# Performance work log

Hardware: AMD Instinct MI355X
Metric: run time of the kernel (lower is better)

## Reference

```python
import jax, jax.numpy as jnp
import numpy as np

N = 500000   # num instances
C = 64       # num clock regions (8x8 grid)
CHIP_W, CHIP_H = 168.0, 480.0


def setup_inputs() -> dict:
    key = jax.random.key(0)
    k1, k2, k3 = jax.random.split(key, 3)
    # 8x8 grid of clock-region well boxes (xl, yl, xh, yh) tiling the chip
    gx, gy = 8, 8
    cw, ch = CHIP_W / gx, CHIP_H / gy
    ix = np.arange(C) % gx
    iy = np.arange(C) // gx
    well_boxes = jnp.asarray(
        np.stack([ix * cw, iy * ch, (ix + 1) * cw, (iy + 1) * ch], axis=1),
        dtype=jnp.float32)
    # instance centers uniformly over the chip
    inst_pos = jax.random.uniform(k1, (N, 2), dtype=jnp.float32) * jnp.array(
        [CHIP_W, CHIP_H], dtype=jnp.float32)
    # half sizes in [0.25, 0.75) sites (module stores inst_sizes * 0.5)
    half_inst_sizes = jax.random.uniform(k2, (N, 2), dtype=jnp.float32) * 0.5 + 0.25
    inst_areas = 4.0 * half_inst_sizes[:, 0] * half_inst_sizes[:, 1]
    # per-instance candidate CR availability; guarantee >=1 available CR
    avail = jax.random.randint(k3, (N, C), 0, 2) > 0
    avail = avail.at[:, 0].set(True)
    exponents = jnp.full((N,), 2.0, dtype=jnp.float32)
    return {
        'inst_pos': inst_pos,
        'half_inst_sizes': half_inst_sizes,
        'inst_areas': inst_areas,
        'well_boxes': well_boxes,
        'inst_cr_avail_map': avail,
        'exponents': exponents,
    }


def reference(inst_pos, half_inst_sizes, inst_areas, well_boxes,
              inst_cr_avail_map, exponents):
    # Per-instance CR selection + box-overlap well energy.
    x = inst_pos[:, 0:1]           # (N,1)
    y = inst_pos[:, 1:2]
    hx = half_inst_sizes[:, 0:1]
    hy = half_inst_sizes[:, 1:2]
    xl, yl, xh, yh = (well_boxes[:, 0], well_boxes[:, 1],
                      well_boxes[:, 2], well_boxes[:, 3])  # each (C,)
    # protrusion distance of the instance box outside each well box, (N,C)
    dx = jnp.maximum(jnp.maximum(xl - (x - hx), (x + hx) - xh), 0.0)
    dy = jnp.maximum(jnp.maximum(yl - (y - hy), (y + hy) - yh), 0.0)
    dist = dx + dy
    # mask out unavailable clock regions, pick nearest available CR
    dist = jnp.where(inst_cr_avail_map, dist, jnp.inf)
    selected_crs = jnp.argmin(dist, axis=1)  # (N,)
    dx_sel = jnp.take_along_axis(dx, selected_crs[:, None], axis=1)[:, 0]
    dy_sel = jnp.take_along_axis(dy, selected_crs[:, None], axis=1)[:, 0]
    # per-instance exponentiated well energy
    energy = jnp.power(dx_sel, exponents) + jnp.power(dy_sel, exponents)
    return energy
```

## Files before the change

### kernel.cpp

```cpp
#include <hip/hip_runtime.h>
#include <stdint.h>


#define C_WELLS 64

__global__ __launch_bounds__(256, 8)
void energy_well_kernel(const float* __restrict__ inst_pos,
                        const float* __restrict__ half_sizes,
                        const float* __restrict__ well_boxes,
                        const int*   __restrict__ avail,
                        const float* __restrict__ exponents,
                        float* __restrict__ out,
                        int N)
{
    const int lane = threadIdx.x & 63;
    int waveId = __builtin_amdgcn_readfirstlane(
        (int)((blockIdx.x * blockDim.x + threadIdx.x) >> 6));
    const int nWaves = (gridDim.x * blockDim.x) >> 6;

    const float4 box = ((const float4*)well_boxes)[lane];

    for (int i = waveId; i < N; i += nWaves) {
        const float x  = inst_pos[2 * i];
        const float y  = inst_pos[2 * i + 1];
        const float hx = half_sizes[2 * i];
        const float hy = half_sizes[2 * i + 1];
        const float e  = exponents[i];
        const int av = avail[(size_t)i * C_WELLS + lane];

        const float dx = fmaxf(fmaxf(box.x - (x - hx), (x + hx) - box.z), 0.0f);
        const float dy = fmaxf(fmaxf(box.y - (y - hy), (y + hy) - box.w), 0.0f);
        float dist = dx + dy;
        dist = av ? dist : __builtin_inff();

        float m = dist;
        #pragma unroll
        for (int off = 32; off >= 1; off >>= 1)
            m = fminf(m, __shfl_xor(m, off, 64));

        unsigned long long eq = __ballot(dist == m);
        const int w = __ffsll((long long)eq) - 1;

        const float dxs = __shfl(dx, w, 64);
        const float dys = __shfl(dy, w, 64);

        if (lane == 0) {
            float energy;
            if (e == 2.0f) {
                energy = dxs * dxs + dys * dys;
            } else {
                energy = powf(dxs, e) + powf(dys, e);
            }
            out[i] = energy;
        }
    }
}

extern "C" void kernel_launch(void* const* d_in, const int* in_sizes, int n_in,
                              void* d_out, int out_size, void* d_ws, size_t ws_size,
                              hipStream_t stream)
{
    const float* inst_pos   = (const float*)d_in[0];
    const float* half_sizes = (const float*)d_in[1];
    const float* well_boxes = (const float*)d_in[3];
    const int*   avail      = (const int*)d_in[4];
    const float* exponents  = (const float*)d_in[5];
    float* out = (float*)d_out;

    const int N = in_sizes[5];

    const int blocks = 2048;
    energy_well_kernel<<<dim3(blocks), dim3(256), 0, stream>>>(
        inst_pos, half_sizes, well_boxes, avail, exponents, out, N);
}
```

Before: 242.2 us.

## Process 64 instances per wave with ballot-packed availability masks

Switches from one instance per wave with cross-lane min reduction to one instance per lane, with each wave handling a tile of 64 instances. Availability rows are read coalesced and packed into per-lane 64-bit masks via ballot, then each lane scans all wells serially from broadcast box loads. This is meant to remove the per-instance shuffle reduction and serialized latency, increasing memory-level parallelism on the large availability array, at the cost of more per-lane ALU work.

After: 225.3 us. -7.0%, faster.

```diff
diff --git a/kernel.cpp b/kernel.cpp
--- a/kernel.cpp
+++ b/kernel.cpp
@@ -7,50 +7,65 @@
 __global__ __launch_bounds__(256, 8)
 void energy_well_kernel(const float* __restrict__ inst_pos,
                         const float* __restrict__ half_sizes,
-                        const float* __restrict__ well_boxes,
+                        const float4* __restrict__ well_boxes,
                         const int*   __restrict__ avail,
                         const float* __restrict__ exponents,
                         float* __restrict__ out,
-                        int N)
+                        int N, int nTiles)
 {
     const int lane = threadIdx.x & 63;
-    int waveId = __builtin_amdgcn_readfirstlane(
-        (int)((blockIdx.x * blockDim.x + threadIdx.x) >> 6));
+    const int waveId = (int)((blockIdx.x * blockDim.x + threadIdx.x) >> 6);
     const int nWaves = (gridDim.x * blockDim.x) >> 6;
 
-    const float4 box = ((const float4*)well_boxes)[lane];
+    for (int tile = waveId; tile < nTiles; tile += nWaves) {
+        const int base = tile << 6;
+        const int i    = base + lane;
 
-    for (int i = waveId; i < N; i += nWaves) {
-        const float x  = inst_pos[2 * i];
-        const float y  = inst_pos[2 * i + 1];
-        const float hx = half_sizes[2 * i];
-        const float hy = half_sizes[2 * i + 1];
-        const float e  = exponents[i];
-        const int av = avail[(size_t)i * C_WELLS + lane];
+        unsigned long long myMask = 0ull;
+        if (base + C_WELLS <= N) {
+            #pragma unroll 16
+            for (int j = 0; j < C_WELLS; ++j) {
+                const int av = avail[(size_t)(base + j) * C_WELLS + lane];
+                const unsigned long long m = __ballot(av != 0);
+                if (lane == j) myMask = m;
+            }
+        } else {
+            #pragma unroll 16
+            for (int j = 0; j < C_WELLS; ++j) {
+                int av = 0;
+                if (base + j < N) av = avail[(size_t)(base + j) * C_WELLS + lane];
+                const unsigned long long m = __ballot(av != 0);
+                if (lane == j) myMask = m;
+            }
+        }
 
-        const float dx = fmaxf(fmaxf(box.x - (x - hx), (x + hx) - box.z), 0.0f);
-        const float dy = fmaxf(fmaxf(box.y - (y - hy), (y + hy) - box.w), 0.0f);
-        float dist = dx + dy;
-        dist = av ? dist : __builtin_inff();
+        float x = 0.f, y = 0.f, hx = 0.f, hy = 0.f, e = 2.0f;
+        if (i < N) {
+            const float2 p = ((const float2*)inst_pos)[i];
+            const float2 h = ((const float2*)half_sizes)[i];
+            x = p.x; y = p.y; hx = h.x; hy = h.y;
+            e = exponents[i];
+        }
+        const float xm = x - hx, xp = x + hx;
+        const float ym = y - hy, yp = y + hy;
 
-        float m = dist;
+        float best = __builtin_inff();
+        float bdx = 0.0f, bdy = 0.0f;
         #pragma unroll
-        for (int off = 32; off >= 1; off >>= 1)
-            m = fminf(m, __shfl_xor(m, off, 64));
+        for (int c = 0; c < C_WELLS; ++c) {
+            const float4 box = well_boxes[c];
+            const float dx = fmaxf(fmaxf(box.x - xm, xp - box.z), 0.0f);
+            const float dy = fmaxf(fmaxf(box.y - ym, yp - box.w), 0.0f);
+            float dist = dx + dy;
+            const bool av = (myMask >> c) & 1ull;
+            dist = av ? dist : __builtin_inff();
+            if (dist < best) { best = dist; bdx = dx; bdy = dy; }
+        }
 
-        unsigned long long eq = __ballot(dist == m);
-        const int w = __ffsll((long long)eq) - 1;
-
-        const float dxs = __shfl(dx, w, 64);
-        const float dys = __shfl(dy, w, 64);
-
-        if (lane == 0) {
+        if (i < N) {
             float energy;
-            if (e == 2.0f) {
-                energy = dxs * dxs + dys * dys;
-            } else {
-                energy = powf(dxs, e) + powf(dys, e);
-            }
+            if (e == 2.0f) energy = bdx * bdx + bdy * bdy;
+            else           energy = powf(bdx, e) + powf(bdy, e);
             out[i] = energy;
         }
     }
@@ -60,16 +75,18 @@
                               void* d_out, int out_size, void* d_ws, size_t ws_size,
                               hipStream_t stream)
 {
-    const float* inst_pos   = (const float*)d_in[0];
-    const float* half_sizes = (const float*)d_in[1];
-    const float* well_boxes = (const float*)d_in[3];
-    const int*   avail      = (const int*)d_in[4];
-    const float* exponents  = (const float*)d_in[5];
+    const float*  inst_pos   = (const float*)d_in[0];
+    const float*  half_sizes = (const float*)d_in[1];
+    const float4* well_boxes = (const float4*)d_in[3];
+    const int*    avail      = (const int*)d_in[4];
+    const float*  exponents  = (const float*)d_in[5];
     float* out = (float*)d_out;
 
     const int N = in_sizes[5];
+    const int nTiles = (N + C_WELLS - 1) / C_WELLS;
+    const int wavesNeeded = nTiles;
+    const int blocks = (wavesNeeded + 3) / 4;
 
-    const int blocks = 2048;
     energy_well_kernel<<<dim3(blocks), dim3(256), 0, stream>>>(
-        inst_pos, half_sizes, well_boxes, avail, exponents, out, N);
+        inst_pos, half_sizes, well_boxes, avail, exponents, out, N, nTiles);
 }
```

## Process 16 instances per wave with vector avail loads and prefetch

Applied to the files above, without the earlier changes.

Each wave now handles 16 instances per tile, with 4 lanes per instance. Each lane loads 16 availability flags as four int4 loads and does a serial argmin over its 16 regions. A 4-lane shuffle reduction on a packed (distance, lane) key then picks the first minimum, replacing the 64-wide shuffle reduction per instance. The next tile's data is prefetched into registers while the current tile is computed. Grid size and occupancy hint are halved. The bandwidth-bound avail read becomes wider and is overlapped with compute, at the cost of more registers and a well-box layout hardcoded for the 8x8 grid.

New measurement: 199.2 us. -17.8%, faster.

```diff
diff --git a/kernel.cpp b/kernel.cpp
--- a/kernel.cpp
+++ b/kernel.cpp
@@ -4,55 +4,120 @@
 
 #define C_WELLS 64
 
-__global__ __launch_bounds__(256, 8)
-void energy_well_kernel(const float* __restrict__ inst_pos,
-                        const float* __restrict__ half_sizes,
-                        const float* __restrict__ well_boxes,
-                        const int*   __restrict__ avail,
-                        const float* __restrict__ exponents,
+struct TileWork {
+    int4   av[4];
+    float2 p, h;
+    float  e;
+};
+
+__device__ __forceinline__ TileWork load_tile(
+    const int4* __restrict__ avail4, const float2* __restrict__ inst_pos,
+    const float2* __restrict__ half_sizes, const float* __restrict__ exponents,
+    int tile, int lane, int N)
+{
+    TileWork w;
+    const int i  = tile * 16 + (lane >> 2);
+    const int ii = i < N ? i : N - 1;
+    const int4* a = avail4 + ((size_t)ii * 16 + (size_t)(lane & 3) * 4);
+    w.av[0] = a[0]; w.av[1] = a[1]; w.av[2] = a[2]; w.av[3] = a[3];
+    w.p = inst_pos[ii];
+    w.h = half_sizes[ii];
+    w.e = exponents[ii];
+    return w;
+}
+
+__global__ __launch_bounds__(256, 4)
+void energy_well_kernel(const float2* __restrict__ inst_pos,
+                        const float2* __restrict__ half_sizes,
+                        const float*  __restrict__ well_boxes,
+                        const int4*   __restrict__ avail4,
+                        const float*  __restrict__ exponents,
                         float* __restrict__ out,
-                        int N)
+                        int N, int nT16)
 {
     const int lane = threadIdx.x & 63;
-    int waveId = __builtin_amdgcn_readfirstlane(
-        (int)((blockIdx.x * blockDim.x + threadIdx.x) >> 6));
+    const int sub  = lane & 3;
+    const int waveId = (int)((blockIdx.x * blockDim.x + threadIdx.x) >> 6);
     const int nWaves = (gridDim.x * blockDim.x) >> 6;
 
-    const float4 box = ((const float4*)well_boxes)[lane];
+    float xlv[8], xhv[8];
+    #pragma unroll
+    for (int ix = 0; ix < 8; ++ix) {
+        xlv[ix] = well_boxes[4 * ix + 0];
+        xhv[ix] = well_boxes[4 * ix + 2];
+    }
+    const float ylA = well_boxes[64 * sub + 1];
+    const float yhA = well_boxes[64 * sub + 3];
+    const float ylB = well_boxes[64 * sub + 33];
+    const float yhB = well_boxes[64 * sub + 35];
 
-    for (int i = waveId; i < N; i += nWaves) {
-        const float x  = inst_pos[2 * i];
-        const float y  = inst_pos[2 * i + 1];
-        const float hx = half_sizes[2 * i];
-        const float hy = half_sizes[2 * i + 1];
-        const float e  = exponents[i];
-        const int av = avail[(size_t)i * C_WELLS + lane];
+    int tile = waveId;
+    if (tile >= nT16) return;
 
-        const float dx = fmaxf(fmaxf(box.x - (x - hx), (x + hx) - box.z), 0.0f);
-        const float dy = fmaxf(fmaxf(box.y - (y - hy), (y + hy) - box.w), 0.0f);
-        float dist = dx + dy;
-        dist = av ? dist : __builtin_inff();
+    TileWork w = load_tile(avail4, inst_pos, half_sizes, exponents, tile, lane, N);
 
-        float m = dist;
+    while (true) {
+        const int nt = tile + nWaves;
+        TileWork wn;
+        const bool more = nt < nT16;
+        if (more)
+            wn = load_tile(avail4, inst_pos, half_sizes, exponents, nt, lane, N);
+
+        const float xm = w.p.x - w.h.x, xp_ = w.p.x + w.h.x;
+        const float ym = w.p.y - w.h.y, yp_ = w.p.y + w.h.y;
+
+        float dxv[8];
         #pragma unroll
-        for (int off = 32; off >= 1; off >>= 1)
-            m = fminf(m, __shfl_xor(m, off, 64));
+        for (int ix = 0; ix < 8; ++ix)
+            dxv[ix] = fmaxf(fmaxf(xlv[ix] - xm, xp_ - xhv[ix]), 0.0f);
+        const float dyA = fmaxf(fmaxf(ylA - ym, yp_ - yhA), 0.0f);
+        const float dyB = fmaxf(fmaxf(ylB - ym, yp_ - yhB), 0.0f);
 
-        unsigned long long eq = __ballot(dist == m);
-        const int w = __ffsll((long long)eq) - 1;
+        float best = __builtin_inff();
+        float bdx = 0.0f, bdy = 0.0f;
+        #pragma unroll
+        for (int j = 0; j < 4; ++j) {
+            const int4 a4 = w.av[j];
+            #pragma unroll
+            for (int k = 0; k < 4; ++k) {
+                const int c2 = 4 * j + k;
+                const int av = (k == 0) ? a4.x : (k == 1) ? a4.y
+                             : (k == 2) ? a4.z : a4.w;
+                const int   ix = c2 & 7;
+                const float dy = (c2 < 8) ? dyA : dyB;
+                const float dist = dxv[ix] + dy;
+                const bool upd = (av != 0) && (dist < best);
+                best = upd ? dist    : best;
+                bdx  = upd ? dxv[ix] : bdx;
+                bdy  = upd ? dy      : bdy;
+            }
+        }
 
-        const float dxs = __shfl(dx, w, 64);
-        const float dys = __shfl(dy, w, 64);
+        const unsigned kb  = __float_as_uint(best);
+        unsigned klo = (kb << 2) | (unsigned)sub;
+        unsigned khi = kb >> 30;
+        const unsigned mylo = klo, myhi = khi;
+        #pragma unroll
+        for (int off = 1; off <= 2; off <<= 1) {
+            const unsigned plo = __shfl_xor(klo, off, 64);
+            const unsigned phi = __shfl_xor(khi, off, 64);
+            const bool less = (phi < khi) || (phi == khi && plo < klo);
+            klo = less ? plo : klo;
+            khi = less ? phi : khi;
+        }
+        const bool winner = (khi == myhi) && (klo == mylo);
 
-        if (lane == 0) {
+        const int i = tile * 16 + (lane >> 2);
+        if (winner && i < N) {
             float energy;
-            if (e == 2.0f) {
-                energy = dxs * dxs + dys * dys;
-            } else {
-                energy = powf(dxs, e) + powf(dys, e);
-            }
+            if (w.e == 2.0f) energy = bdx * bdx + bdy * bdy;
+            else             energy = powf(bdx, w.e) + powf(bdy, w.e);
             out[i] = energy;
         }
+
+        if (!more) break;
+        w = wn;
+        tile = nt;
     }
 }
 
@@ -60,16 +125,17 @@
                               void* d_out, int out_size, void* d_ws, size_t ws_size,
                               hipStream_t stream)
 {
-    const float* inst_pos   = (const float*)d_in[0];
-    const float* half_sizes = (const float*)d_in[1];
-    const float* well_boxes = (const float*)d_in[3];
-    const int*   avail      = (const int*)d_in[4];
-    const float* exponents  = (const float*)d_in[5];
+    const float2* inst_pos   = (const float2*)d_in[0];
+    const float2* half_sizes = (const float2*)d_in[1];
+    const float*  well_boxes = (const float*)d_in[3];
+    const int4*   avail4     = (const int4*)d_in[4];
+    const float*  exponents  = (const float*)d_in[5];
     float* out = (float*)d_out;
 
     const int N = in_sizes[5];
+    const int nT16 = (N + 15) / 16;
 
-    const int blocks = 2048;
+    const int blocks = 1024;
     energy_well_kernel<<<dim3(blocks), dim3(256), 0, stream>>>(
-        inst_pos, half_sizes, well_boxes, avail, exponents, out, N);
+        inst_pos, half_sizes, well_boxes, avail4, exponents, out, N, nT16);
 }
```
